# Optimization experiments

Measured on AMD Instinct MI355X. Metric: run time of the kernel, lower is better.

Reference implementation:

```python
import jax, jax.numpy as jnp
import numpy as np

B, H, W, C = 4, 128, 128, 192
NH, WS, SS = 6, 16, 8
N = WS * WS
HD = C // NH
SCALE = HD ** -0.5
CONV_SCALE = 0.01


def _win_part(x, ws):
    b, h, w, c = x.shape
    x = x.reshape(b, h // ws, ws, w // ws, ws, c).transpose(0, 1, 3, 2, 4, 5)
    return x.reshape(-1, ws * ws, c)


def _win_rev(win, ws, h, w):
    b = win.shape[0] // ((h // ws) * (w // ws))
    x = win.reshape(b, h // ws, w // ws, ws, ws, -1).transpose(0, 1, 3, 2, 4, 5)
    return x.reshape(b, h, w, -1)


def _ln(x, g, b):
    m = x.mean(-1, keepdims=True)
    v = x.var(-1, keepdims=True)
    return (x - m) * jax.lax.rsqrt(v + 1e-5) * g + b


def _conv3(x, w, b):
    return jax.lax.conv_general_dilated(x, w, (1, 1), 'SAME', dimension_numbers=('NHWC', 'HWIO', 'NHWC')) + b


def _rpi_sa(ws):
    coords = np.stack(np.meshgrid(np.arange(ws), np.arange(ws), indexing='ij'))
    cf = coords.reshape(2, -1)
    rc = (cf[:, :, None] - cf[:, None, :]).transpose(1, 2, 0).copy()
    rc[:, :, 0] += ws - 1
    rc[:, :, 1] += ws - 1
    rc[:, :, 0] *= 2 * ws - 1
    return rc.sum(-1)


def _attn_mask(h, w, ws, ss):
    img = np.zeros((1, h, w, 1), dtype=np.float32)
    slices = (slice(0, -ws), slice(-ws, -ss), slice(-ss, None))
    cnt = 0
    for hs in slices:
        for wsl in slices:
            img[:, hs, wsl, :] = cnt
            cnt += 1
    mw = img.reshape(1, h // ws, ws, w // ws, ws, 1).transpose(0, 1, 3, 2, 4, 5).reshape(-1, ws * ws)
    am = mw[:, None, :] - mw[:, :, None]
    return np.where(am != 0, -100.0, 0.0).astype(np.float32)


def setup_inputs() -> dict:
    key = jax.random.key(0)
    ks = jax.random.split(key, 10)
    std = 0.02
    return {
        'x': jax.random.normal(ks[0], (B, H * W, C), jnp.float32),
        'qkv_w': jax.random.normal(ks[1], (C, 3 * C), jnp.float32) * std,
        'qkv_b': jnp.zeros((3 * C,), jnp.float32),
        'proj_w': jax.random.normal(ks[2], (C, C), jnp.float32) * std,
        'proj_b': jnp.zeros((C,), jnp.float32),
        'rpb': jax.random.normal(ks[3], ((2 * WS - 1) ** 2, NH), jnp.float32) * std,
        'norm1_w': jnp.ones((C,), jnp.float32),
        'norm1_b': jnp.zeros((C,), jnp.float32),
        'norm2_w': jnp.ones((C,), jnp.float32),
        'norm2_b': jnp.zeros((C,), jnp.float32),
        'conv1_w': jax.random.normal(ks[4], (3, 3, C, C // 3), jnp.float32) * std,
        'conv1_b': jnp.zeros((C // 3,), jnp.float32),
        'conv2_w': jax.random.normal(ks[5], (3, 3, C // 3, C), jnp.float32) * std,
        'conv2_b': jnp.zeros((C,), jnp.float32),
        'ca1_w': jax.random.normal(ks[6], (C, C // 30), jnp.float32) * std,
        'ca1_b': jnp.zeros((C // 30,), jnp.float32),
        'ca2_w': jax.random.normal(ks[7], (C // 30, C), jnp.float32) * std,
        'ca2_b': jnp.zeros((C,), jnp.float32),
        'fc1_w': jax.random.normal(ks[8], (C, 4 * C), jnp.float32) * std,
        'fc1_b': jnp.zeros((4 * C,), jnp.float32),
        'fc2_w': jax.random.normal(ks[9], (4 * C, C), jnp.float32) * std,
        'fc2_b': jnp.zeros((C,), jnp.float32),
        'rpi': jnp.asarray(_rpi_sa(WS), jnp.int32),
        'attn_mask': jnp.asarray(_attn_mask(H, W, WS, SS)),
    }


def reference(x, qkv_w, qkv_b, proj_w, proj_b, rpb, norm1_w, norm1_b, norm2_w, norm2_b,
              conv1_w, conv1_b, conv2_w, conv2_b, ca1_w, ca1_b, ca2_w, ca2_b,
              fc1_w, fc1_b, fc2_w, fc2_b, rpi, attn_mask):
    b = x.shape[0]
    shortcut = x
    xn = _ln(x, norm1_w, norm1_b).reshape(b, H, W, C)

    # CAB conv branch: conv3x3 -> GELU -> conv3x3 -> channel attention
    cv = jax.nn.gelu(_conv3(xn, conv1_w, conv1_b), approximate=False)
    cv = _conv3(cv, conv2_w, conv2_b)
    pooled = cv.mean(axis=(1, 2))                                  # [b, C] global avg pool
    ca = jax.nn.sigmoid(jnp.maximum(pooled @ ca1_w + ca1_b, 0.0) @ ca2_w + ca2_b)
    conv_x = (cv * ca[:, None, None, :]).reshape(b, H * W, C)

    # shifted window attention
    shifted = jnp.roll(xn, (-SS, -SS), axis=(1, 2))
    xw = _win_part(shifted, WS)                                    # [b*nw, N, C]
    b_ = xw.shape[0]
    qkv = (xw @ qkv_w + qkv_b).reshape(b_, N, 3, NH, HD).transpose(2, 0, 3, 1, 4)
    q, k, v = qkv[0] * SCALE, qkv[1], qkv[2]                       # [b_, NH, N, HD]
    attn = jnp.einsum('whnd,whmd->whnm', q, k)                     # [b_, NH, N, N]
    bias = rpb[rpi.reshape(-1)].reshape(N, N, NH).transpose(2, 0, 1)
    attn = attn + bias[None]
    nw = attn_mask.shape[0]
    attn = attn.reshape(b, nw, NH, N, N) + attn_mask[None, :, None]
    attn = jax.nn.softmax(attn, axis=-1).reshape(b_, NH, N, N)
    out = jnp.einsum('whnm,whmd->whnd', attn, v).transpose(0, 2, 1, 3).reshape(b_, N, C)
    out = out @ proj_w + proj_b
    rev = _win_rev(out, WS, H, W)
    attn_x = jnp.roll(rev, (SS, SS), axis=(1, 2)).reshape(b, H * W, C)

    y = shortcut + attn_x + conv_x * CONV_SCALE

    # MLP
    yn = _ln(y, norm2_w, norm2_b)
    mlp = jax.nn.gelu(yn @ fc1_w + fc1_b, approximate=False) @ fc2_w + fc2_b
    return y + mlp
```

## Files before the change

kernel.cpp:

```cpp
#include <hip/hip_runtime.h>
#include <hip/hip_bf16.h>
#include <cstdint>
#include <cstddef>

#define BB 4
#define CC 192
#define NHEAD 6
#define WSZ 16
#define SSH 8
#define NTOK 256
#define HD 32
#define HWPIX 16384
#define TTOT 65536
#define WWID 128
#define SCALE_Q 0.17677669529663687f
#define CONV_SC 0.01f
#define PSTR 264
#define KSTR 40

typedef __hip_bfloat16 bf16;
typedef __attribute__((ext_vector_type(8))) short short8;
typedef __attribute__((ext_vector_type(4))) float float4v;

__device__ __forceinline__ float b2f(bf16 v) { return __bfloat162float(v); }
__device__ __forceinline__ bf16 f2b(float v) { return __float2bfloat16(v); }
__device__ __forceinline__ unsigned short f2bu(float f) {
  bf16 h = __float2bfloat16(f);
  return *reinterpret_cast<unsigned short*>(&h);
}
__device__ __forceinline__ float gelu_exact(float x) {
  return 0.5f * x * (1.0f + erff(x * 0.7071067811865475f));
}
__device__ __forceinline__ short8 ld8z(const bf16* p, bool ok) {
  if (ok) return *(const short8*)p;
  short8 z = {0, 0, 0, 0, 0, 0, 0, 0};
  return z;
}
__device__ __forceinline__ void glds16(const void* g, void* l) {
  __builtin_amdgcn_global_load_lds(
      (const __attribute__((address_space(1))) unsigned int*)g,
      (__attribute__((address_space(3))) unsigned int*)l, 16, 0, 0);
}

__global__ __launch_bounds__(256) void k_ln1(const float* __restrict__ x,
                                             const float* __restrict__ g,
                                             const float* __restrict__ b,
                                             bf16* __restrict__ xn) {
  int wv = threadIdx.x >> 6, lane = threadIdx.x & 63;
  int tok = blockIdx.x * 4 + wv;
  size_t row = (size_t)tok * CC;
  float v0 = x[row + lane], v1 = x[row + lane + 64], v2 = x[row + lane + 128];
  float s = v0 + v1 + v2, ss = v0 * v0 + v1 * v1 + v2 * v2;
#pragma unroll
  for (int off = 1; off < 64; off <<= 1) {
    s += __shfl_xor(s, off, 64);
    ss += __shfl_xor(ss, off, 64);
  }
  float mean = s * (1.0f / CC);
  float rstd = rsqrtf(ss * (1.0f / CC) - mean * mean + 1e-5f);
  xn[row + lane]       = f2b((v0 - mean) * rstd * g[lane]       + b[lane]);
  xn[row + lane + 64]  = f2b((v1 - mean) * rstd * g[lane + 64]  + b[lane + 64]);
  xn[row + lane + 128] = f2b((v2 - mean) * rstd * g[lane + 128] + b[lane + 128]);
}

__global__ __launch_bounds__(256) void k_biasq(const int* __restrict__ rpi,
                                               const float* __restrict__ rpb,
                                               float* __restrict__ biasQ) {
  int k = threadIdx.x;
  int h = blockIdx.x >> 8;
  int q = blockIdx.x & 255;
  biasQ[(size_t)blockIdx.x * 256 + ((k & 15) << 4) + (k >> 4)] =
      rpb[rpi[q * 256 + k] * NHEAD + h];
}

__global__ __launch_bounds__(256) void k_wprep(const float* __restrict__ c1w,
                                               const float* __restrict__ c2w,
                                               bf16* __restrict__ wT1,
                                               bf16* __restrict__ wT2) {
  int i = blockIdx.x * 256 + threadIdx.x;
  {
    int tap = i / (64 * 192); int r = i % (64 * 192);
    int oc = r / 192, ci = r % 192;
    wT1[i] = f2b(c1w[(size_t)(tap * 192 + ci) * 64 + oc]);
  }
  {
    int tap = i / (192 * 64); int r = i % (192 * 64);
    int oc = r / 64, ci = r % 64;
    wT2[i] = f2b(c2w[(size_t)(tap * 64 + ci) * 192 + oc]);
  }
}

__global__ __launch_bounds__(256) void k_wprep2(const float* __restrict__ fc1w,
                                                const float* __restrict__ fc2w,
                                                bf16* __restrict__ wF1,
                                                bf16* __restrict__ wF2) {
  int i = blockIdx.x * 256 + threadIdx.x;
  {
    int n = i / 192, k = i % 192;
    wF1[i] = f2b(fc1w[(size_t)k * 768 + n]);
  }
  {
    int n = i / 768, k = i % 768;
    wF2[i] = f2b(fc2w[(size_t)k * 192 + n]);
  }
}

__global__ __launch_bounds__(256) void k_wprep3(const float* __restrict__ qkvw,
                                                const float* __restrict__ projw,
                                                bf16* __restrict__ wQv,
                                                bf16* __restrict__ wP) {
  int i = blockIdx.x * 256 + threadIdx.x;
  if (i < 576 * 192) {
    int n = i / 192, k = i % 192;
    wQv[i] = f2b(qkvw[(size_t)k * 576 + n]);
  }
  if (i < 192 * 192) {
    int n = i / 192, k = i % 192;
    wP[i] = f2b(projw[(size_t)k * 192 + n]);
  }
}

__global__ __launch_bounds__(256) void k_qkvg2(const bf16* __restrict__ xn,
                                               const bf16* __restrict__ wQv,
                                               const float* __restrict__ qb,
                                               bf16* __restrict__ Qg,
                                               bf16* __restrict__ Kg,
                                               bf16* __restrict__ Vg) {
  int tok0 = blockIdx.x * 32;
  int wave = threadIdx.x >> 6, lane = threadIdx.x & 63;
  int lm = lane & 15, lq = lane >> 4;
  const bf16* arow0 = xn + (size_t)(tok0 + lm) * CC + lq * 8;
  const bf16* arow1 = xn + (size_t)(tok0 + 16 + lm) * CC + lq * 8;
  float4v acc[9][2];
#pragma unroll
  for (int nt = 0; nt < 9; ++nt)
#pragma unroll
    for (int tt = 0; tt < 2; ++tt) acc[nt][tt] = (float4v){0.f, 0.f, 0.f, 0.f};
#pragma unroll
  for (int ks = 0; ks < 6; ++ks) {
    short8 af0 = *(const short8*)(arow0 + ks * 32);
    short8 af1 = *(const short8*)(arow1 + ks * 32);
#pragma unroll
    for (int nt = 0; nt < 9; ++nt) {
      int col = wave * 144 + nt * 16 + lm;
      short8 bfrag = *(const short8*)(wQv + (size_t)col * CC + ks * 32 + lq * 8);
      acc[nt][0] = __builtin_amdgcn_mfma_f32_16x16x32_bf16(af0, bfrag, acc[nt][0], 0, 0, 0);
      acc[nt][1] = __builtin_amdgcn_mfma_f32_16x16x32_bf16(af1, bfrag, acc[nt][1], 0, 0, 0);
    }
  }
  size_t base[2][4];
#pragma unroll
  for (int tt = 0; tt < 2; ++tt)
#pragma unroll
    for (int reg = 0; reg < 4; ++reg) {
      int tg = tok0 + tt * 16 + lq * 4 + reg;
      int b = tg >> 14;
      int pix = tg & 16383;
      int gh = pix >> 7, gw = pix & 127;
      int hs = (gh + 120) & 127, wsx = (gw + 120) & 127;
      int wdx = (b << 6) + ((hs >> 4) << 3) + (wsx >> 4);
      int ndx = ((hs & 15) << 4) + (wsx & 15);
      base[tt][reg] = ((size_t)wdx * NHEAD) * NTOK * HD + (size_t)ndx * HD;
    }
#pragma unroll
  for (int nt = 0; nt < 9; ++nt) {
    int col = wave * 144 + nt * 16 + lm;
    float bias = qb[col];
    int sect = col / 192, within = col - sect * 192;
    int head = within >> 5, d = within & 31;
    bf16* dst = (sect == 0) ? Qg : (sect == 1) ? Kg : Vg;
    float scale = (sect == 0) ? SCALE_Q : 1.f;
#pragma unroll
    for (int tt = 0; tt < 2; ++tt)
#pragma unroll
      for (int reg = 0; reg < 4; ++reg) {
        dst[base[tt][reg] + (size_t)head * NTOK * HD + d] =
            f2b((acc[nt][tt][reg] + bias) * scale);
      }
  }
}

__global__ __launch_bounds__(256) void k_attn3(const bf16* __restrict__ Qg,
                                               const bf16* __restrict__ Kg,
                                               const bf16* __restrict__ Vg,
                                               const float* __restrict__ biasP,
                                               bf16* __restrict__ AO) {
  __shared__ unsigned short PTw[4][16 * PSTR];
  __shared__ unsigned short VT[32 * PSTR];
  __shared__ unsigned short KL[256 * KSTR];
  int wh = blockIdx.x >> 1, half = blockIdx.x & 1;
  int wdx = wh / NHEAD, h = wh - wdx * NHEAD;
  int wl = wdx & 63;
  int wr = wl >> 3, wc = wl & 7;
  int tid = threadIdx.x;
  int wave = tid >> 6, lane = tid & 63;
  int lm = lane & 15, lq = lane >> 4;
  int q0 = half * 128;
  bool needmask = (wr == 7) || (wc == 7);

  {
    const uint4* vp = (const uint4*)(Vg + ((size_t)wh * NTOK + tid) * HD);
    uint4 vv[4] = {vp[0], vp[1], vp[2], vp[3]};
    const uint4* kp = (const uint4*)(Kg + ((size_t)wh * NTOK + tid) * HD);
    uint4 kv[4] = {kp[0], kp[1], kp[2], kp[3]};
#pragma unroll
    for (int i = 0; i < 4; ++i) {
      unsigned arr[4] = {vv[i].x, vv[i].y, vv[i].z, vv[i].w};
#pragma unroll
      for (int j = 0; j < 4; ++j) {
        int d = i * 8 + j * 2;
        VT[d * PSTR + tid]       = (unsigned short)(arr[j] & 0xffffu);
        VT[(d + 1) * PSTR + tid] = (unsigned short)(arr[j] >> 16);
      }
      *(uint4*)&KL[tid * KSTR + i * 8] = kv[i];
    }
  }
  __syncthreads();

  int wsk = (wc << 4) + lm;
  int ridk_w = (wsk >= 112) + (wsk >= 120);
  unsigned short* PT = &PTw[wave][0];

  float4v oacc[2][2];
#pragma unroll
  for (int rt = 0; rt < 2; ++rt)
#pragma unroll
    for (int c2 = 0; c2 < 2; ++c2) oacc[rt][c2] = (float4v){0.f, 0.f, 0.f, 0.f};
  float linv[2][4];

#pragma unroll
  for (int rt = 0; rt < 2; ++rt) {
    int qrow = q0 + wave * 32 + rt * 16;
    short8 aq = *(const short8*)(Qg + ((size_t)wh * NTOK + qrow + lm) * HD + lq * 8);
    float4v sacc[16];
#pragma unroll
    for (int ct = 0; ct < 16; ++ct) sacc[ct] = (float4v){0.f, 0.f, 0.f, 0.f};
#pragma unroll
    for (int ct = 0; ct < 16; ++ct) {
      short8 kf = *(const short8*)&KL[(ct * 16 + lm) * KSTR + lq * 8];
      sacc[ct] = __builtin_amdgcn_mfma_f32_16x16x32_bf16(aq, kf, sacc[ct], 0, 0, 0);
    }
#pragma unroll
    for (int reg = 0; reg < 4; ++reg) {
      int nq = qrow + lq * 4 + reg;
      const float* bp = biasP + ((size_t)(h * 256 + nq)) * 256 + lm * 16;
      float bb[16];
      *(float4*)&bb[0]  = ((const float4*)bp)[0];
      *(float4*)&bb[4]  = ((const float4*)bp)[1];
      *(float4*)&bb[8]  = ((const float4*)bp)[2];
      *(float4*)&bb[12] = ((const float4*)bp)[3];
      float sv[16];
      float mx = -1.0e30f;
      if (needmask) {
        int hsq = (wr << 4) + (nq >> 4), wsq = (wc << 4) + (nq & 15);
        int ridq = ((hsq >= 112) + (hsq >= 120)) * 3 + ((wsq >= 112) + (wsq >= 120));
#pragma unroll
        for (int ct = 0; ct < 16; ++ct) {
          int hsk = (wr << 4) + ct;
          int ridk = ((hsk >= 112) + (hsk >= 120)) * 3 + ridk_w;
          float s = sacc[ct][reg] + bb[ct] + ((ridk != ridq) ? -100.f : 0.f);
          sv[ct] = s;
          mx = fmaxf(mx, s);
        }
      } else {
#pragma unroll
        for (int ct = 0; ct < 16; ++ct) {
          float s = sacc[ct][reg] + bb[ct];
          sv[ct] = s;
          mx = fmaxf(mx, s);
        }
      }
#pragma unroll
      for (int off = 1; off < 16; off <<= 1) mx = fmaxf(mx, __shfl_xor(mx, off, 64));
      float l = 0.f;
#pragma unroll
      for (int ct = 0; ct < 16; ++ct) {
        float p = __expf(sv[ct] - mx);
        l += p;
        PT[(lq * 4 + reg) * PSTR + ct * 16 + lm] = f2bu(p);
      }
#pragma unroll
      for (int off = 1; off < 16; off <<= 1) l += __shfl_xor(l, off, 64);
      linv[rt][reg] = 1.f / l;
    }
#pragma unroll
    for (int kb = 0; kb < 8; ++kb) {
      short8 pf = *(const short8*)&PT[lm * PSTR + kb * 32 + lq * 8];
#pragma unroll
      for (int c2 = 0; c2 < 2; ++c2) {
        short8 vf = *(const short8*)&VT[(c2 * 16 + lm) * PSTR + kb * 32 + lq * 8];
        oacc[rt][c2] = __builtin_amdgcn_mfma_f32_16x16x32_bf16(pf, vf, oacc[rt][c2], 0, 0, 0);
      }
    }
  }
#pragma unroll
  for (int rt = 0; rt < 2; ++rt)
#pragma unroll
    for (int c2 = 0; c2 < 2; ++c2) {
      int d = c2 * 16 + lm;
#pragma unroll
      for (int reg = 0; reg < 4; ++reg) {
        int nq = q0 + wave * 32 + rt * 16 + lq * 4 + reg;
        AO[((size_t)wdx * NTOK + nq) * CC + h * HD + d] =
            f2b(oacc[rt][c2][reg] * linv[rt][reg]);
      }
    }
}

__global__ __launch_bounds__(256) void k_proj2(const bf16* __restrict__ AO,
                                               const bf16* __restrict__ wP,
                                               const float* __restrict__ pb,
                                               const float* __restrict__ x,
                                               float* __restrict__ y) {
  int r0 = blockIdx.x * 32;
  int wave = threadIdx.x >> 6, lane = threadIdx.x & 63;
  int lm = lane & 15, lq = lane >> 4;
  const bf16* arow0 = AO + (size_t)(r0 + lm) * CC + lq * 8;
  const bf16* arow1 = AO + (size_t)(r0 + 16 + lm) * CC + lq * 8;
  float4v acc[3][2];
#pragma unroll
  for (int nt = 0; nt < 3; ++nt)
#pragma unroll
    for (int tt = 0; tt < 2; ++tt) acc[nt][tt] = (float4v){0.f, 0.f, 0.f, 0.f};
#pragma unroll
  for (int ks = 0; ks < 6; ++ks) {
    short8 af0 = *(const short8*)(arow0 + ks * 32);
    short8 af1 = *(const short8*)(arow1 + ks * 32);
#pragma unroll
    for (int nt = 0; nt < 3; ++nt) {
      int col = wave * 48 + nt * 16 + lm;
      short8 bfrag = *(const short8*)(wP + (size_t)col * CC + ks * 32 + lq * 8);
      acc[nt][0] = __builtin_amdgcn_mfma_f32_16x16x32_bf16(af0, bfrag, acc[nt][0], 0, 0, 0);
      acc[nt][1] = __builtin_amdgcn_mfma_f32_16x16x32_bf16(af1, bfrag, acc[nt][1], 0, 0, 0);
    }
  }
  size_t drow[2][4];
#pragma unroll
  for (int tt = 0; tt < 2; ++tt)
#pragma unroll
    for (int reg = 0; reg < 4; ++reg) {
      int r = r0 + tt * 16 + lq * 4 + reg;
      int wdx = r >> 8, n = r & 255;
      int wb = wdx >> 6, wl = wdx & 63;
      int hs = ((wl >> 3) << 4) + (n >> 4);
      int wsx = ((wl & 7) << 4) + (n & 15);
      int gh = (hs + SSH) & 127, gw = (wsx + SSH) & 127;
      drow[tt][reg] = ((size_t)wb * HWPIX + (size_t)gh * WWID + gw) * CC;
    }
#pragma unroll
  for (int nt = 0; nt < 3; ++nt) {
    int col = wave * 48 + nt * 16 + lm;
    float bias = pb[col];
#pragma unroll
    for (int tt = 0; tt < 2; ++tt)
#pragma unroll
      for (int reg = 0; reg < 4; ++reg) {
        y[drow[tt][reg] + col] = x[drow[tt][reg] + col] + acc[nt][tt][reg] + bias;
      }
  }
}

__global__ __launch_bounds__(512, 1) void k_conv1l(const bf16* __restrict__ xn,
                                                   const bf16* __restrict__ wT1,
                                                   const float* __restrict__ c1b,
                                                   bf16* __restrict__ cv1) {
  __shared__ unsigned short xs[3 * 128 * 192];
  int hh = blockIdx.x & 127, b = blockIdx.x >> 7;
  int tid = threadIdx.x;
  int wave = tid >> 6, lane = tid & 63;
  int lm = lane & 15, lq = lane >> 4;
  int ph = wave >> 2;
  int oc = (wave & 3) * 16 + lm;

#pragma unroll
  for (int r = 0; r < 3; ++r) {
    int gh = hh + r - 1;
    if ((unsigned)gh < 128u) {
      const char* src = (const char*)(xn + (size_t)(b * HWPIX + gh * WWID) * CC);
#pragma unroll
      for (int j = 0; j < 6; ++j) {
        int c = j * 512 + tid;
        int px = c / 24, kc = c - px * 24;
        glds16(src + (size_t)px * 384 + ((size_t)(kc ^ (px & 7)) << 4),
               (char*)xs + ((size_t)(r * 3072 + j * 512 + wave * 64)) * 16);
      }
    }
  }
  __syncthreads();

  float4v acc[4];
#pragma unroll
  for (int t = 0; t < 4; ++t) acc[t] = (float4v){0.f, 0.f, 0.f, 0.f};

  short8 w[6], wn[6];
#pragma unroll
  for (int ks = 0; ks < 6; ++ks)
    w[ks] = *(const short8*)(wT1 + ((size_t)oc) * CC + ks * 32 + lq * 8);
#pragma unroll
  for (int tap = 0; tap < 9; ++tap) {
    if (tap < 8) {
#pragma unroll
      for (int ks = 0; ks < 6; ++ks)
        wn[ks] = *(const short8*)(wT1 + ((size_t)((tap + 1) * 64) + oc) * CC + ks * 32 + lq * 8);
    }
    int kh = tap / 3, kw = tap % 3;
    int gh = hh + kh - 1;
    if ((unsigned)gh < 128u) {
      const unsigned short* row = &xs[kh * 24576];
#pragma unroll
      for (int ks = 0; ks < 6; ++ks) {
#pragma unroll
        for (int t = 0; t < 4; ++t) {
          int px = ph * 64 + t * 16 + lm + kw - 1;
          int pxc = px < 0 ? 0 : (px > 127 ? 127 : px);
          short8 av = *(const short8*)&row[pxc * 192 + (((ks * 4 + lq) ^ (pxc & 7)) << 3)];
          short8 zz = {0, 0, 0, 0, 0, 0, 0, 0};
          short8 a = ((unsigned)px < 128u) ? av : zz;
          acc[t] = __builtin_amdgcn_mfma_f32_16x16x32_bf16(a, w[ks], acc[t], 0, 0, 0);
        }
      }
    }
#pragma unroll
    for (int ks = 0; ks < 6; ++ks) w[ks] = wn[ks];
  }
  float bias = c1b[oc];
#pragma unroll
  for (int t = 0; t < 4; ++t) {
    int pxb = ph * 64 + t * 16 + lq * 4;
    size_t base = ((size_t)b * HWPIX + (size_t)hh * WWID + pxb) * 64 + oc;
    cv1[base]       = f2b(gelu_exact(acc[t][0] + bias));
    cv1[base + 64]  = f2b(gelu_exact(acc[t][1] + bias));
    cv1[base + 128] = f2b(gelu_exact(acc[t][2] + bias));
    cv1[base + 192] = f2b(gelu_exact(acc[t][3] + bias));
  }
}

__global__ __launch_bounds__(512, 2) void k_conv2l(const bf16* __restrict__ cv1,
                                                   const bf16* __restrict__ wT2,
                                                   const float* __restrict__ c2b,
                                                   bf16* __restrict__ cv2) {
  __shared__ unsigned short cs[3 * 128 * 64];
  int hh = blockIdx.x & 127, b = blockIdx.x >> 7;
  int tid = threadIdx.x;
  int wave = tid >> 6, lane = tid & 63;
  int lm = lane & 15, lq = lane >> 4;
  int ph = wave >> 2;
  int og = wave & 3;

#pragma unroll
  for (int r = 0; r < 3; ++r) {
    int gh = hh + r - 1;
    if ((unsigned)gh < 128u) {
      const char* src = (const char*)(cv1 + (size_t)(b * HWPIX + gh * WWID) * 64);
#pragma unroll
      for (int j = 0; j < 2; ++j) {
        int c = j * 512 + tid;
        int px = c >> 3, kc = c & 7;
        glds16(src + (size_t)px * 128 + ((size_t)(kc ^ (px & 7)) << 4),
               (char*)cs + ((size_t)(r * 1024 + j * 512 + wave * 64)) * 16);
      }
    }
  }
  __syncthreads();

  float4v acc[3][4];
#pragma unroll
  for (int nt = 0; nt < 3; ++nt)
#pragma unroll
    for (int t = 0; t < 4; ++t) acc[nt][t] = (float4v){0.f, 0.f, 0.f, 0.f};

  short8 w[3][2], wn[3][2];
#pragma unroll
  for (int nt = 0; nt < 3; ++nt) {
    int oc = og * 48 + nt * 16 + lm;
#pragma unroll
    for (int ks = 0; ks < 2; ++ks)
      w[nt][ks] = *(const short8*)(wT2 + ((size_t)oc) * 64 + ks * 32 + lq * 8);
  }
#pragma unroll
  for (int tap = 0; tap < 9; ++tap) {
    if (tap < 8) {
#pragma unroll
      for (int nt = 0; nt < 3; ++nt) {
        int oc = og * 48 + nt * 16 + lm;
#pragma unroll
        for (int ks = 0; ks < 2; ++ks)
          wn[nt][ks] = *(const short8*)(wT2 + ((size_t)((tap + 1) * 192) + oc) * 64 + ks * 32 + lq * 8);
      }
    }
    int kh = tap / 3, kw = tap % 3;
    int gh = hh + kh - 1;
    if ((unsigned)gh < 128u) {
      const unsigned short* row = &cs[kh * 8192];
#pragma unroll
      for (int ks = 0; ks < 2; ++ks) {
#pragma unroll
        for (int t = 0; t < 4; ++t) {
          int px = ph * 64 + t * 16 + lm + kw - 1;
          int pxc = px < 0 ? 0 : (px > 127 ? 127 : px);
          short8 av = *(const short8*)&row[pxc * 64 + (((ks * 4 + lq) ^ (pxc & 7)) << 3)];
          short8 zz = {0, 0, 0, 0, 0, 0, 0, 0};
          short8 a = ((unsigned)px < 128u) ? av : zz;
#pragma unroll
          for (int nt = 0; nt < 3; ++nt)
            acc[nt][t] = __builtin_amdgcn_mfma_f32_16x16x32_bf16(a, w[nt][ks], acc[nt][t], 0, 0, 0);
        }
      }
    }
#pragma unroll
    for (int nt = 0; nt < 3; ++nt)
#pragma unroll
      for (int ks = 0; ks < 2; ++ks) w[nt][ks] = wn[nt][ks];
  }
#pragma unroll
  for (int nt = 0; nt < 3; ++nt) {
    int oc = og * 48 + nt * 16 + lm;
    float bias = c2b[oc];
#pragma unroll
    for (int t = 0; t < 4; ++t) {
      int pxb = ph * 64 + t * 16 + lq * 4;
      size_t base = ((size_t)b * HWPIX + (size_t)hh * WWID + pxb) * CC + oc;
      cv2[base]           = f2b(acc[nt][t][0] + bias);
      cv2[base + CC]      = f2b(acc[nt][t][1] + bias);
      cv2[base + 2 * CC]  = f2b(acc[nt][t][2] + bias);
      cv2[base + 3 * CC]  = f2b(acc[nt][t][3] + bias);
    }
  }
}

__global__ __launch_bounds__(192) void k_pool(const bf16* __restrict__ cv2,
                                              float* __restrict__ pooled) {
  int t = threadIdx.x;
  int b = blockIdx.x >> 7;
  int pc = blockIdx.x & 127;
  const bf16* base = cv2 + ((size_t)b * HWPIX + (size_t)pc * 128) * CC + t;
  float s = 0.f;
#pragma unroll 4
  for (int p = 0; p < 128; ++p) s += b2f(base[(size_t)p * CC]);
  atomicAdd(&pooled[b * CC + t], s);
}

__global__ __launch_bounds__(192) void k_ca(const float* __restrict__ pooled,
                                            const float* __restrict__ w1,
                                            const float* __restrict__ b1,
                                            const float* __restrict__ w2,
                                            const float* __restrict__ b2,
                                            float* __restrict__ ca) {
  __shared__ float pld[CC];
  __shared__ float t1[6];
  int t = threadIdx.x, b = blockIdx.x;
  pld[t] = pooled[b * CC + t] * (1.0f / HWPIX);
  __syncthreads();
  if (t < 6) {
    float s = b1[t];
    for (int c = 0; c < CC; ++c) s += pld[c] * w1[c * 6 + t];
    t1[t] = fmaxf(s, 0.f);
  }
  __syncthreads();
  float s = b2[t];
#pragma unroll
  for (int k = 0; k < 6; ++k) s += t1[k] * w2[k * CC + t];
  ca[b * CC + t] = 1.f / (1.f + __expf(-s));
}

__global__ __launch_bounds__(256) void k_ln2(const float* __restrict__ y,
                                             const bf16* __restrict__ cv2,
                                             const float* __restrict__ ca,
                                             const float* __restrict__ g2,
                                             const float* __restrict__ b2,
                                             bf16* __restrict__ yn) {
  int wv = threadIdx.x >> 6, lane = threadIdx.x & 63;
  int tok = blockIdx.x * 4 + wv;
  const float* cab = ca + (tok >> 14) * CC;
  size_t row = (size_t)tok * CC;
  float v0 = y[row + lane]       + b2f(cv2[row + lane])       * cab[lane]       * CONV_SC;
  float v1 = y[row + lane + 64]  + b2f(cv2[row + lane + 64])  * cab[lane + 64]  * CONV_SC;
  float v2 = y[row + lane + 128] + b2f(cv2[row + lane + 128]) * cab[lane + 128] * CONV_SC;
  float s = v0 + v1 + v2, ss = v0 * v0 + v1 * v1 + v2 * v2;
#pragma unroll
  for (int off = 1; off < 64; off <<= 1) {
    s += __shfl_xor(s, off, 64);
    ss += __shfl_xor(ss, off, 64);
  }
  float mean = s * (1.0f / CC);
  float rstd = rsqrtf(ss * (1.0f / CC) - mean * mean + 1e-5f);
  yn[row + lane]       = f2b((v0 - mean) * rstd * g2[lane]       + b2[lane]);
  yn[row + lane + 64]  = f2b((v1 - mean) * rstd * g2[lane + 64]  + b2[lane + 64]);
  yn[row + lane + 128] = f2b((v2 - mean) * rstd * g2[lane + 128] + b2[lane + 128]);
}

__global__ __launch_bounds__(256, 2) void k_fc1ws(const bf16* __restrict__ yn,
                                                  const bf16* __restrict__ wF1,
                                                  const float* __restrict__ fb1,
                                                  bf16* __restrict__ h) {
  __shared__ unsigned short wl[192 * 192];
  int cg = blockIdx.x & 3, tb = blockIdx.x >> 2;
  int tid = threadIdx.x;
  int wave = tid >> 6, lane = tid & 63;
  int lm = lane & 15, lq = lane >> 4;

  const char* src = (const char*)wF1 + (size_t)cg * 73728;
#pragma unroll
  for (int j = 0; j < 18; ++j) {
    int ci = j * 256 + tid;
    int r = ci / 24, c = ci - r * 24;
    glds16(src + (size_t)r * 384 + ((c ^ (r & 7)) << 4),
           (char*)wl + (size_t)(j * 256 + wave * 64) * 16);
  }
  __syncthreads();

  short8 wfr[3][6];
#pragma unroll
  for (int nt = 0; nt < 3; ++nt) {
    int rl = wave * 48 + nt * 16 + lm;
#pragma unroll
    for (int ks = 0; ks < 6; ++ks)
      wfr[nt][ks] = *(const short8*)&wl[rl * 192 + (((ks * 4 + lq) ^ (rl & 7)) << 3)];
  }
  float4 b4[3];
#pragma unroll
  for (int nt = 0; nt < 3; ++nt)
    b4[nt] = *(const float4*)(fb1 + cg * 192 + wave * 48 + nt * 16 + lq * 4);

  int tok0b = tb * 512;
#pragma unroll 2
  for (int t = 0; t < 32; ++t) {
    int tok0 = tok0b + t * 16;
    const bf16* arow = yn + (size_t)(tok0 + lm) * CC + lq * 8;
    float4v acc[3];
#pragma unroll
    for (int nt = 0; nt < 3; ++nt) acc[nt] = (float4v){0.f, 0.f, 0.f, 0.f};
#pragma unroll
    for (int ks = 0; ks < 6; ++ks) {
      short8 tf = *(const short8*)(arow + ks * 32);
#pragma unroll
      for (int nt = 0; nt < 3; ++nt)
        acc[nt] = __builtin_amdgcn_mfma_f32_16x16x32_bf16(wfr[nt][ks], tf, acc[nt], 0, 0, 0);
    }
    bf16* hrow = h + (size_t)(tok0 + lm) * 768 + cg * 192 + wave * 48 + lq * 4;
#pragma unroll
    for (int nt = 0; nt < 3; ++nt) {
      unsigned short u0 = f2bu(gelu_exact(acc[nt][0] + b4[nt].x));
      unsigned short u1 = f2bu(gelu_exact(acc[nt][1] + b4[nt].y));
      unsigned short u2 = f2bu(gelu_exact(acc[nt][2] + b4[nt].z));
      unsigned short u3 = f2bu(gelu_exact(acc[nt][3] + b4[nt].w));
      uint2 pk;
      pk.x = (unsigned)u0 | ((unsigned)u1 << 16);
      pk.y = (unsigned)u2 | ((unsigned)u3 << 16);
      *(uint2*)(hrow + nt * 16) = pk;
    }
  }
}

__global__ __launch_bounds__(256, 2) void k_fc2m(const bf16* __restrict__ h,
                                                 const bf16* __restrict__ wF2,
                                                 const float* __restrict__ fb2,
                                                 const float* __restrict__ y,
                                                 const bf16* __restrict__ cv2,
                                                 const float* __restrict__ ca,
                                                 float* __restrict__ out) {
  __shared__ unsigned short ha[2][4096];
  __shared__ unsigned short wbt[2][6144];
  int r0 = blockIdx.x * 128;
  int tid = threadIdx.x;
  int wave = tid >> 6, lane = tid & 63;
  int lm = lane & 15, lq = lane >> 4;

  const char* hsrc = (const char*)(h + (size_t)r0 * 768);
  const char* wsrc = (const char*)wF2;

  float4v acc[2][12];
#pragma unroll
  for (int mt = 0; mt < 2; ++mt)
#pragma unroll
    for (int nt = 0; nt < 12; ++nt) acc[mt][nt] = (float4v){0.f, 0.f, 0.f, 0.f};

  auto stage = [&](int kc, int b) {
    int k0b = kc * 64;
#pragma unroll
    for (int j = 0; j < 2; ++j) {
      int c = j * 256 + tid;
      glds16(hsrc + (size_t)(c >> 2) * 1536 + k0b + (c & 3) * 16,
             (char*)&ha[b][0] + (j * 256 + wave * 64) * 16);
    }
#pragma unroll
    for (int j = 0; j < 3; ++j) {
      int c = j * 256 + tid;
      glds16(wsrc + (size_t)(c >> 2) * 1536 + k0b + (c & 3) * 16,
             (char*)&wbt[b][0] + (j * 256 + wave * 64) * 16);
    }
  };

  stage(0, 0);
  __syncthreads();
#pragma unroll 1
  for (int kc = 0; kc < 24; ++kc) {
    int cur = kc & 1;
    if (kc < 23) stage(kc + 1, cur ^ 1);
    short8 af[2], bf[12];
#pragma unroll
    for (int mt = 0; mt < 2; ++mt)
      af[mt] = *(const short8*)&ha[cur][(wave * 32 + mt * 16 + lm) * 32 + lq * 8];
#pragma unroll
    for (int nt = 0; nt < 12; ++nt)
      bf[nt] = *(const short8*)&wbt[cur][(nt * 16 + lm) * 32 + lq * 8];
#pragma unroll
    for (int mt = 0; mt < 2; ++mt)
#pragma unroll
      for (int nt = 0; nt < 12; ++nt)
        acc[mt][nt] = __builtin_amdgcn_mfma_f32_16x16x32_bf16(af[mt], bf[nt], acc[mt][nt], 0, 0, 0);
    __syncthreads();
  }

  const float* cab = ca + (r0 >> 14) * CC;
#pragma unroll
  for (int nt = 0; nt < 12; ++nt) {
    int col = nt * 16 + lm;
    float bias = fb2[col];
    float cas = cab[col] * CONV_SC;
#pragma unroll
    for (int mt = 0; mt < 2; ++mt) {
#pragma unroll
      for (int reg = 0; reg < 4; ++reg) {
        int tok = r0 + wave * 32 + mt * 16 + lq * 4 + reg;
        size_t idx = (size_t)tok * CC + col;
        out[idx] = y[idx] + b2f(cv2[idx]) * cas + acc[mt][nt][reg] + bias;
      }
    }
  }
}

extern "C" void kernel_launch(void* const* d_in, const int* in_sizes, int n_in,
                              void* d_out, int out_size, void* d_ws, size_t ws_size,
                              hipStream_t stream) {
  const float* x      = (const float*)d_in[0];
  const float* qkv_w  = (const float*)d_in[1];
  const float* qkv_b  = (const float*)d_in[2];
  const float* proj_w = (const float*)d_in[3];
  const float* proj_b = (const float*)d_in[4];
  const float* rpb    = (const float*)d_in[5];
  const float* n1w    = (const float*)d_in[6];
  const float* n1b    = (const float*)d_in[7];
  const float* n2w    = (const float*)d_in[8];
  const float* n2b    = (const float*)d_in[9];
  const float* c1w    = (const float*)d_in[10];
  const float* c1b    = (const float*)d_in[11];
  const float* c2w    = (const float*)d_in[12];
  const float* c2b    = (const float*)d_in[13];
  const float* ca1w   = (const float*)d_in[14];
  const float* ca1b   = (const float*)d_in[15];
  const float* ca2w   = (const float*)d_in[16];
  const float* ca2b   = (const float*)d_in[17];
  const float* fc1w   = (const float*)d_in[18];
  const float* fc1b   = (const float*)d_in[19];
  const float* fc2w   = (const float*)d_in[20];
  const float* fc2b   = (const float*)d_in[21];
  const int*   rpi    = (const int*)d_in[22];
  (void)in_sizes; (void)n_in; (void)out_size; (void)ws_size;

  char* wsb = (char*)d_ws;
  bf16*  xn    = (bf16*)(wsb + 0);
  bf16*  yn    = (bf16*)(wsb + 0);
  float* biasQ = (float*)(wsb + 25165824);
  bf16*  Qg    = (bf16*)(wsb + 26738688);
  bf16*  Kg    = (bf16*)(wsb + 51904512);
  bf16*  Vg    = (bf16*)(wsb + 77070336);
  bf16*  AO    = (bf16*)(wsb + 102236160);
  bf16*  hbuf  = (bf16*)(wsb + 26738688);
  float* y     = (float*)(wsb + 127401984);
  bf16*  cv1   = (bf16*)(wsb + 177733632);
  bf16*  cv2   = (bf16*)(wsb + 186122240);
  float* pool  = (float*)(wsb + 211288064);
  float* cavec = (float*)(wsb + 211291136);
  bf16*  wT1   = (bf16*)(wsb + 211294208);
  bf16*  wT2   = (bf16*)(wsb + 211515392);
  bf16*  wF1   = (bf16*)(wsb + 211736576);
  bf16*  wF2   = (bf16*)(wsb + 212031488);
  bf16*  wQv   = (bf16*)(wsb + 212326400);
  bf16*  wP    = (bf16*)(wsb + 212547584);
  float* out   = (float*)d_out;

  k_ln1<<<TTOT / 4, 256, 0, stream>>>(x, n1w, n1b, xn);
  k_biasq<<<NHEAD * NTOK, 256, 0, stream>>>(rpi, rpb, biasQ);
  k_wprep<<<432, 256, 0, stream>>>(c1w, c2w, wT1, wT2);
  k_wprep2<<<576, 256, 0, stream>>>(fc1w, fc2w, wF1, wF2);
  k_wprep3<<<576, 256, 0, stream>>>(qkv_w, proj_w, wQv, wP);
  k_qkvg2<<<TTOT / 32, 256, 0, stream>>>(xn, wQv, qkv_b, Qg, Kg, Vg);
  k_attn3<<<BB * 64 * NHEAD * 2, 256, 0, stream>>>(Qg, Kg, Vg, biasQ, AO);
  k_proj2<<<TTOT / 32, 256, 0, stream>>>(AO, wP, proj_b, x, y);
  k_conv1l<<<BB * 128, 512, 0, stream>>>(xn, wT1, c1b, cv1);
  k_conv2l<<<BB * 128, 512, 0, stream>>>(cv1, wT2, c2b, cv2);
  hipMemsetAsync(pool, 0, BB * CC * sizeof(float), stream);
  k_pool<<<512, 192, 0, stream>>>(cv2, pool);
  k_ca<<<BB, 192, 0, stream>>>(pool, ca1w, ca1b, ca2w, ca2b, cavec);
  k_ln2<<<TTOT / 4, 256, 0, stream>>>(y, cv2, cavec, n2w, n2b, yn);
  k_fc1ws<<<512, 256, 0, stream>>>(yn, wF1, fc1b, hbuf);
  k_fc2m<<<512, 256, 0, stream>>>(hbuf, wF2, fc2b, y, cv2, cavec, out);
}
```

Before: 561.7 us.

## Make QKV and projection GEMMs weight-stationary with LDS-staged register-resident weights

The QKV and output-projection GEMMs are restructured into persistent weight-stationary kernels. Each block loads a 192x192 weight slice into swizzled LDS once, keeps it in registers as MFMA fragments, and loops over 512 tokens in 16-token steps. The MFMA operands are swapped so each lane holds four consecutive output columns, which allows packed 8-byte bf16 stores and float4 residual loads and stores. This removes repeated global weight-fragment reads per 32-token tile but cuts the grid to 384 and 128 blocks, which risks underfilling the GPU, especially for the projection.

```diff
diff --git a/kernel.cpp b/kernel.cpp
--- a/kernel.cpp
+++ b/kernel.cpp
@@ -120,63 +120,83 @@
   }
 }
 
-__global__ __launch_bounds__(256) void k_qkvg2(const bf16* __restrict__ xn,
-                                               const bf16* __restrict__ wQv,
-                                               const float* __restrict__ qb,
-                                               bf16* __restrict__ Qg,
-                                               bf16* __restrict__ Kg,
-                                               bf16* __restrict__ Vg) {
-  int tok0 = blockIdx.x * 32;
-  int wave = threadIdx.x >> 6, lane = threadIdx.x & 63;
+__global__ __launch_bounds__(256, 2) void k_qkvws(const bf16* __restrict__ xn,
+                                                  const bf16* __restrict__ wQv,
+                                                  const float* __restrict__ qb,
+                                                  bf16* __restrict__ Qg,
+                                                  bf16* __restrict__ Kg,
+                                                  bf16* __restrict__ Vg) {
+  __shared__ unsigned short wl[192 * 192];
+  int cg = blockIdx.x / 128, tb = blockIdx.x - cg * 128;
+  int tid = threadIdx.x;
+  int wave = tid >> 6, lane = tid & 63;
   int lm = lane & 15, lq = lane >> 4;
-  const bf16* arow0 = xn + (size_t)(tok0 + lm) * CC + lq * 8;
-  const bf16* arow1 = xn + (size_t)(tok0 + 16 + lm) * CC + lq * 8;
-  float4v acc[9][2];
-#pragma unroll
-  for (int nt = 0; nt < 9; ++nt)
-#pragma unroll
-    for (int tt = 0; tt < 2; ++tt) acc[nt][tt] = (float4v){0.f, 0.f, 0.f, 0.f};
-#pragma unroll
-  for (int ks = 0; ks < 6; ++ks) {
-    short8 af0 = *(const short8*)(arow0 + ks * 32);
-    short8 af1 = *(const short8*)(arow1 + ks * 32);
-#pragma unroll
-    for (int nt = 0; nt < 9; ++nt) {
-      int col = wave * 144 + nt * 16 + lm;
-      short8 bfrag = *(const short8*)(wQv + (size_t)col * CC + ks * 32 + lq * 8);
-      acc[nt][0] = __builtin_amdgcn_mfma_f32_16x16x32_bf16(af0, bfrag, acc[nt][0], 0, 0, 0);
-      acc[nt][1] = __builtin_amdgcn_mfma_f32_16x16x32_bf16(af1, bfrag, acc[nt][1], 0, 0, 0);
-    }
-  }
-  size_t base[2][4];
-#pragma unroll
-  for (int tt = 0; tt < 2; ++tt)
-#pragma unroll
-    for (int reg = 0; reg < 4; ++reg) {
-      int tg = tok0 + tt * 16 + lq * 4 + reg;
-      int b = tg >> 14;
-      int pix = tg & 16383;
-      int gh = pix >> 7, gw = pix & 127;
-      int hs = (gh + 120) & 127, wsx = (gw + 120) & 127;
-      int wdx = (b << 6) + ((hs >> 4) << 3) + (wsx >> 4);
-      int ndx = ((hs & 15) << 4) + (wsx & 15);
-      base[tt][reg] = ((size_t)wdx * NHEAD) * NTOK * HD + (size_t)ndx * HD;
-    }
-#pragma unroll
-  for (int nt = 0; nt < 9; ++nt) {
-    int col = wave * 144 + nt * 16 + lm;
-    float bias = qb[col];
-    int sect = col / 192, within = col - sect * 192;
-    int head = within >> 5, d = within & 31;
-    bf16* dst = (sect == 0) ? Qg : (sect == 1) ? Kg : Vg;
-    float scale = (sect == 0) ? SCALE_Q : 1.f;
-#pragma unroll
-    for (int tt = 0; tt < 2; ++tt)
-#pragma unroll
-      for (int reg = 0; reg < 4; ++reg) {
-        dst[base[tt][reg] + (size_t)head * NTOK * HD + d] =
-            f2b((acc[nt][tt][reg] + bias) * scale);
-      }
+
+  const char* src = (const char*)wQv + (size_t)cg * 73728;
+#pragma unroll
+  for (int j = 0; j < 18; ++j) {
+    int ci = j * 256 + tid;
+    int r = ci / 24, c = ci - r * 24;
+    glds16(src + (size_t)r * 384 + ((c ^ (r & 7)) << 4),
+           (char*)wl + (size_t)(j * 256 + wave * 64) * 16);
+  }
+  __syncthreads();
+
+  short8 wfr[3][6];
+#pragma unroll
+  for (int nt = 0; nt < 3; ++nt) {
+    int rl = wave * 48 + nt * 16 + lm;
+#pragma unroll
+    for (int ks = 0; ks < 6; ++ks)
+      wfr[nt][ks] = *(const short8*)&wl[rl * 192 + (((ks * 4 + lq) ^ (rl & 7)) << 3)];
+  }
+  float4 b4[3];
+  int head[3], d0[3];
+#pragma unroll
+  for (int nt = 0; nt < 3; ++nt) {
+    int n0p = wave * 48 + nt * 16 + lq * 4;
+    b4[nt] = *(const float4*)(qb + cg * 192 + n0p);
+    head[nt] = n0p >> 5;
+    d0[nt] = n0p & 31;
+  }
+  bf16* dst = (cg == 0) ? Qg : (cg == 1) ? Kg : Vg;
+  float scale = (cg == 0) ? SCALE_Q : 1.f;
+
+  int tok0b = tb * 512;
+#pragma unroll 2
+  for (int t = 0; t < 32; ++t) {
+    int tok0 = tok0b + t * 16;
+    const bf16* arow = xn + (size_t)(tok0 + lm) * CC + lq * 8;
+    int tg = tok0 + lm;
+    int b = tg >> 14;
+    int pix = tg & 16383;
+    int gh = pix >> 7, gw = pix & 127;
+    int hs = (gh + 120) & 127, wsx = (gw + 120) & 127;
+    int wdx = (b << 6) + ((hs >> 4) << 3) + (wsx >> 4);
+    int ndx = ((hs & 15) << 4) + (wsx & 15);
+    size_t base = ((size_t)wdx * NHEAD) * NTOK * HD + (size_t)ndx * HD;
+
+    float4v acc[3];
+#pragma unroll
+    for (int nt = 0; nt < 3; ++nt) acc[nt] = (float4v){0.f, 0.f, 0.f, 0.f};
+#pragma unroll
+    for (int ks = 0; ks < 6; ++ks) {
+      short8 tf = *(const short8*)(arow + ks * 32);
+#pragma unroll
+      for (int nt = 0; nt < 3; ++nt)
+        acc[nt] = __builtin_amdgcn_mfma_f32_16x16x32_bf16(wfr[nt][ks], tf, acc[nt], 0, 0, 0);
+    }
+#pragma unroll
+    for (int nt = 0; nt < 3; ++nt) {
+      unsigned short u0 = f2bu((acc[nt][0] + b4[nt].x) * scale);
+      unsigned short u1 = f2bu((acc[nt][1] + b4[nt].y) * scale);
+      unsigned short u2 = f2bu((acc[nt][2] + b4[nt].z) * scale);
+      unsigned short u3 = f2bu((acc[nt][3] + b4[nt].w) * scale);
+      uint2 pk;
+      pk.x = (unsigned)u0 | ((unsigned)u1 << 16);
+      pk.y = (unsigned)u2 | ((unsigned)u3 << 16);
+      *(uint2*)(dst + base + (size_t)head[nt] * NTOK * HD + d0[nt]) = pk;
+    }
   }
 }
 
@@ -307,56 +327,74 @@
     }
 }
 
-__global__ __launch_bounds__(256) void k_proj2(const bf16* __restrict__ AO,
-                                               const bf16* __restrict__ wP,
-                                               const float* __restrict__ pb,
-                                               const float* __restrict__ x,
-                                               float* __restrict__ y) {
-  int r0 = blockIdx.x * 32;
-  int wave = threadIdx.x >> 6, lane = threadIdx.x & 63;
+__global__ __launch_bounds__(256, 2) void k_projws(const bf16* __restrict__ AO,
+                                                   const bf16* __restrict__ wP,
+                                                   const float* __restrict__ pb,
+                                                   const float* __restrict__ x,
+                                                   float* __restrict__ y) {
+  __shared__ unsigned short wl[192 * 192];
+  int tb = blockIdx.x;
+  int tid = threadIdx.x;
+  int wave = tid >> 6, lane = tid & 63;
   int lm = lane & 15, lq = lane >> 4;
-  const bf16* arow0 = AO + (size_t)(r0 + lm) * CC + lq * 8;
-  const bf16* arow1 = AO + (size_t)(r0 + 16 + lm) * CC + lq * 8;
-  float4v acc[3][2];
+
+  const char* src = (const char*)wP;
+#pragma unroll
+  for (int j = 0; j < 18; ++j) {
+    int ci = j * 256 + tid;
+    int r = ci / 24, c = ci - r * 24;
+    glds16(src + (size_t)r * 384 + ((c ^ (r & 7)) << 4),
+           (char*)wl + (size_t)(j * 256 + wave * 64) * 16);
+  }
+  __syncthreads();
+
+  short8 wfr[3][6];
+#pragma unroll
+  for (int nt = 0; nt < 3; ++nt) {
+    int rl = wave * 48 + nt * 16 + lm;
+#pragma unroll
+    for (int ks = 0; ks < 6; ++ks)
+      wfr[nt][ks] = *(const short8*)&wl[rl * 192 + (((ks * 4 + lq) ^ (rl & 7)) << 3)];
+  }
+  float4 b4[3];
 #pragma unroll
   for (int nt = 0; nt < 3; ++nt)
-#pragma unroll
-    for (int tt = 0; tt < 2; ++tt) acc[nt][tt] = (float4v){0.f, 0.f, 0.f, 0.f};
-#pragma unroll
-  for (int ks = 0; ks < 6; ++ks) {
-    short8 af0 = *(const short8*)(arow0 + ks * 32);
-    short8 af1 = *(const short8*)(arow1 + ks * 32);
+    b4[nt] = *(const float4*)(pb + wave * 48 + nt * 16 + lq * 4);
+
+  int r0b = tb * 512;
+#pragma unroll 2
+  for (int t = 0; t < 32; ++t) {
+    int r0 = r0b + t * 16;
+    const bf16* arow = AO + (size_t)(r0 + lm) * CC + lq * 8;
+    int r = r0 + lm;
+    int wdx = r >> 8, n = r & 255;
+    int wb = wdx >> 6, wlx = wdx & 63;
+    int hs = ((wlx >> 3) << 4) + (n >> 4);
+    int wsx = ((wlx & 7) << 4) + (n & 15);
+    int gh = (hs + SSH) & 127, gw = (wsx + SSH) & 127;
+    size_t drow = ((size_t)wb * HWPIX + (size_t)gh * WWID + gw) * CC;
+
+    float4v acc[3];
+#pragma unroll
+    for (int nt = 0; nt < 3; ++nt) acc[nt] = (float4v){0.f, 0.f, 0.f, 0.f};
+#pragma unroll
+    for (int ks = 0; ks < 6; ++ks) {
+      short8 tf = *(const short8*)(arow + ks * 32);
+#pragma unroll
+      for (int nt = 0; nt < 3; ++nt)
+        acc[nt] = __builtin_amdgcn_mfma_f32_16x16x32_bf16(wfr[nt][ks], tf, acc[nt], 0, 0, 0);
+    }
 #pragma unroll
     for (int nt = 0; nt < 3; ++nt) {
-      int col = wave * 48 + nt * 16 + lm;
-      short8 bfrag = *(const short8*)(wP + (size_t)col * CC + ks * 32 + lq * 8);
-      acc[nt][0] = __builtin_amdgcn_mfma_f32_16x16x32_bf16(af0, bfrag, acc[nt][0], 0, 0, 0);
-      acc[nt][1] = __builtin_amdgcn_mfma_f32_16x16x32_bf16(af1, bfrag, acc[nt][1], 0, 0, 0);
-    }
-  }
-  size_t drow[2][4];
-#pragma unroll
-  for (int tt = 0; tt < 2; ++tt)
-#pragma unroll
-    for (int reg = 0; reg < 4; ++reg) {
-      int r = r0 + tt * 16 + lq * 4 + reg;
-      int wdx = r >> 8, n = r & 255;
-      int wb = wdx >> 6, wl = wdx & 63;
-      int hs = ((wl >> 3) << 4) + (n >> 4);
-      int wsx = ((wl & 7) << 4) + (n & 15);
-      int gh = (hs + SSH) & 127, gw = (wsx + SSH) & 127;
-      drow[tt][reg] = ((size_t)wb * HWPIX + (size_t)gh * WWID + gw) * CC;
-    }
-#pragma unroll
-  for (int nt = 0; nt < 3; ++nt) {
-    int col = wave * 48 + nt * 16 + lm;
-    float bias = pb[col];
-#pragma unroll
-    for (int tt = 0; tt < 2; ++tt)
-#pragma unroll
-      for (int reg = 0; reg < 4; ++reg) {
-        y[drow[tt][reg] + col] = x[drow[tt][reg] + col] + acc[nt][tt][reg] + bias;
-      }
+      int col0 = wave * 48 + nt * 16 + lq * 4;
+      float4 xv = *(const float4*)(x + drow + col0);
+      float4 ov;
+      ov.x = xv.x + acc[nt][0] + b4[nt].x;
+      ov.y = xv.y + acc[nt][1] + b4[nt].y;
+      ov.z = xv.z + acc[nt][2] + b4[nt].z;
+      ov.w = xv.w + acc[nt][3] + b4[nt].w;
+      *(float4*)(y + drow + col0) = ov;
+    }
   }
 }
 
@@ -785,9 +823,9 @@
   k_wprep<<<432, 256, 0, stream>>>(c1w, c2w, wT1, wT2);
   k_wprep2<<<576, 256, 0, stream>>>(fc1w, fc2w, wF1, wF2);
   k_wprep3<<<576, 256, 0, stream>>>(qkv_w, proj_w, wQv, wP);
-  k_qkvg2<<<TTOT / 32, 256, 0, stream>>>(xn, wQv, qkv_b, Qg, Kg, Vg);
+  k_qkvws<<<384, 256, 0, stream>>>(xn, wQv, qkv_b, Qg, Kg, Vg);
   k_attn3<<<BB * 64 * NHEAD * 2, 256, 0, stream>>>(Qg, Kg, Vg, biasQ, AO);
-  k_proj2<<<TTOT / 32, 256, 0, stream>>>(AO, wP, proj_b, x, y);
+  k_projws<<<128, 256, 0, stream>>>(AO, wP, proj_b, x, y);
   k_conv1l<<<BB * 128, 512, 0, stream>>>(xn, wT1, c1b, cv1);
   k_conv2l<<<BB * 128, 512, 0, stream>>>(cv1, wT2, c2b, cv2);
   hipMemsetAsync(pool, 0, BB * CC * sizeof(float), stream);
```

New measurement: 544.1 us. -3.1%, faster.
